# Kernel tuning notes

Measured on AMD Instinct MI355X. Metric: run time of the kernel, lower is better.

Reference implementation:

```python
import jax, jax.numpy as jnp
import numpy as np

D_MODEL = 1024
N_HEADS = 16
HEAD_DIM = D_MODEL // N_HEADS
THETA = 10000.0
NEG = -1e9


def apply_rope(x, positions, theta=THETA):
    # x: (B, H, S, d), positions: (B, 1, S)
    d = x.shape[-1]
    inv_freq = 1.0 / (theta ** (jnp.arange(0, d, 2, dtype=jnp.float32) / d))  # (d/2,)
    freqs = positions[..., None].astype(jnp.float32) * inv_freq  # (B, 1, S, d/2)
    cos, sin = jnp.cos(freqs), jnp.sin(freqs)
    xr = x.reshape(x.shape[:-1] + (d // 2, 2))
    xe, xo = xr[..., 0], xr[..., 1]
    rot = jnp.stack([xe * cos - xo * sin, xe * sin + xo * cos], axis=-1)
    return rot.reshape(x.shape)


def setup_inputs() -> dict:
    key = jax.random.key(0)
    ks = jax.random.split(key, 5)
    B, S = 2, 2048
    scale = 1.0 / np.sqrt(D_MODEL)
    return {
        "x": jax.random.normal(ks[0], (B, S, D_MODEL), dtype=jnp.float32),
        "wq": jax.random.normal(ks[1], (D_MODEL, D_MODEL), dtype=jnp.float32) * scale,
        "wk": jax.random.normal(ks[2], (D_MODEL, D_MODEL), dtype=jnp.float32) * scale,
        "wv": jax.random.normal(ks[3], (D_MODEL, D_MODEL), dtype=jnp.float32) * scale,
        "wo": jax.random.normal(ks[4], (D_MODEL, D_MODEL), dtype=jnp.float32) * scale,
        "token_positions": jnp.arange(S, dtype=jnp.int64),
    }


def reference(x, wq, wk, wv, wo, token_positions):
    B, S, D = x.shape
    H, d = N_HEADS, HEAD_DIM
    # QKV projections (module does x @ w.T)
    q = (x @ wq.T).reshape(B, S, H, d).transpose(0, 2, 1, 3)  # (B, H, S, d)
    k = (x @ wk.T).reshape(B, S, H, d).transpose(0, 2, 1, 3)
    v = (x @ wv.T).reshape(B, S, H, d).transpose(0, 2, 1, 3)
    pos = jnp.broadcast_to(token_positions[None, :], (B, S))[:, None, :]  # (B, 1, S)
    q = apply_rope(q, pos)
    k = apply_rope(k, pos)
    scores = jnp.einsum("bhqd,bhkd->bhqk", q, k) / jnp.sqrt(jnp.float32(d))
    causal = jnp.tril(jnp.ones((S, S), dtype=bool))
    scores = jnp.where(causal[None, None], scores, NEG)
    attn = jax.nn.softmax(scores, axis=-1)
    out = jnp.einsum("bhqk,bhkd->bhqd", attn, v)
    out = out.transpose(0, 2, 1, 3).reshape(B, S, D)
    return out @ wo.T
```

## Files before the change

### kernel.cpp

```cpp
#include <hip/hip_runtime.h>

typedef __bf16 bf16;
typedef __bf16 bf16x8 __attribute__((ext_vector_type(8)));
typedef __bf16 bf16x4 __attribute__((ext_vector_type(4)));
typedef float f32x4 __attribute__((ext_vector_type(4)));
typedef float f32x16 __attribute__((ext_vector_type(16)));
typedef float fx2 __attribute__((ext_vector_type(2)));

#define DEV static __device__ __forceinline__

constexpr int BB = 2, SS = 2048, DM = 1024, NH = 16, HD = 64;
constexpr int MTOT = BB * SS;
constexpr float LOG2E = 1.4426950408889634f;

constexpr size_t OFF_XB   = 0;
constexpr size_t OFF_WQKV = OFF_XB   + (size_t)MTOT * DM * 2;
constexpr size_t OFF_WO   = OFF_WQKV + (size_t)3 * DM * DM * 2;
constexpr size_t OFF_TAB  = OFF_WO   + (size_t)DM * DM * 2;
constexpr size_t OFF_Q    = OFF_TAB  + (size_t)SS * (HD/2) * 8;
constexpr size_t OFF_K    = OFF_Q    + (size_t)MTOT * DM * 2;
constexpr size_t OFF_VF   = OFF_K    + (size_t)MTOT * DM * 2;
constexpr size_t OFF_AO   = OFF_VF   + (size_t)MTOT * DM * 2;

typedef const __attribute__((address_space(1))) void gas_void;
typedef __attribute__((address_space(3))) void las_void;

DEV void gload16(const bf16* g, bf16* l) {
  __builtin_amdgcn_global_load_lds((gas_void*)g, (las_void*)l, 16, 0, 0);
}

DEV f32x4 mfma16(bf16x8 a, bf16x8 b, f32x4 c) {
  return __builtin_amdgcn_mfma_f32_16x16x32_bf16(a, b, c, 0, 0, 0);
}

DEV f32x16 mfma32(bf16x8 a, bf16x8 b, f32x16 c) {
  return __builtin_amdgcn_mfma_f32_32x32x16_bf16(a, b, c, 0, 0, 0);
}

DEV unsigned pack2(float a, float b) {
  union { bf16 h[2]; unsigned u; } cv;
  cv.h[0] = (bf16)a; cv.h[1] = (bf16)b;
  return cv.u;
}

__global__ void prep_kernel(const float* __restrict__ x, const float* __restrict__ wq,
    const float* __restrict__ wk, const float* __restrict__ wv, const float* __restrict__ wo,
    const int* __restrict__ pos, bf16* __restrict__ xb, bf16* __restrict__ wqkv,
    bf16* __restrict__ wob, fx2* __restrict__ tab) {
  const int NX4 = MTOT * DM / 4;
  const int NW4 = DM * DM / 4;
  const int TOTC = NX4 + 4 * NW4;
  const int NTAB = SS * (HD / 2);
  const int total = TOTC + NTAB;
  for (int i = blockIdx.x * blockDim.x + threadIdx.x; i < total; i += gridDim.x * blockDim.x) {
    if (i < TOTC) {
      const float* src; bf16* dst; int off;
      if (i < NX4) { src = x; dst = xb; off = i; }
      else {
        int i2 = i - NX4; int which = i2 >> 18; off = i2 & (NW4 - 1);
        src = which == 0 ? wq : which == 1 ? wk : which == 2 ? wv : wo;
        dst = which == 0 ? wqkv : which == 1 ? wqkv + DM * DM : which == 2 ? wqkv + 2 * DM * DM : wob;
      }
      float4 v = ((const float4*)src)[off];
      bf16x4 o4 = { (bf16)v.x, (bf16)v.y, (bf16)v.z, (bf16)v.w };
      ((bf16x4*)dst)[off] = o4;
    } else {
      int e = i - TOTC;
      int s = e >> 5, p = e & 31;
      float invf = __builtin_exp2f(-(float)p * (13.287712379549449f / 32.0f));
      float ang = (float)pos[s] * invf;
      fx2 cs; cs.x = cosf(ang); cs.y = sinf(ang);
      tab[e] = cs;
    }
  }
}

DEV void gemm_bt_128(const bf16* __restrict__ A, const bf16* __restrict__ Bw,
                     int rowA0, int rowB0, f32x4 (&acc)[4][4]) {
  __shared__ __align__(16) bf16 lA[128 * 32];
  __shared__ __align__(16) bf16 lB[128 * 32];
  const int t = threadIdx.x, w = t >> 6, lane = t & 63;
  const int wr = w >> 1, wc = w & 1, g = lane >> 4, c = lane & 15;
#pragma unroll
  for (int mi = 0; mi < 4; mi++)
#pragma unroll
    for (int ni = 0; ni < 4; ni++) acc[mi][ni] = (f32x4){0.f, 0.f, 0.f, 0.f};
  const bf16* ga = A + (size_t)(rowA0 + (t >> 2)) * DM + (t & 3) * 8;
  const bf16* gb = Bw + (size_t)(rowB0 + (t >> 2)) * DM + (t & 3) * 8;
  bf16* la = lA + w * 512;
  bf16* lb = lB + w * 512;
  const int arow = wr * 64 + c, brow = wc * 64 + c;
  for (int k0 = 0; k0 < DM; k0 += 32) {
    gload16(ga + k0,            la);
    gload16(ga + k0 + 64 * DM,  la + 2048);
    gload16(gb + k0,            lb);
    gload16(gb + k0 + 64 * DM,  lb + 2048);
    __syncthreads();
    bf16x8 af[4], bf_[4];
#pragma unroll
    for (int mi = 0; mi < 4; mi++) af[mi]  = *(const bf16x8*)(lA + (arow + mi * 16) * 32 + g * 8);
#pragma unroll
    for (int ni = 0; ni < 4; ni++) bf_[ni] = *(const bf16x8*)(lB + (brow + ni * 16) * 32 + g * 8);
#pragma unroll
    for (int mi = 0; mi < 4; mi++)
#pragma unroll
      for (int ni = 0; ni < 4; ni++)
        acc[mi][ni] = mfma16(af[mi], bf_[ni], acc[mi][ni]);
    __syncthreads();
  }
}

__global__ __launch_bounds__(256, 2) void qkv_kernel(const bf16* __restrict__ xb,
    const bf16* __restrict__ wqkv, const fx2* __restrict__ tab,
    bf16* __restrict__ Qb, bf16* __restrict__ Kb, bf16* __restrict__ VFb) {
  f32x4 acc[4][4];
  const int rowA0 = blockIdx.y * 128, rowB0 = blockIdx.x * 128;
  gemm_bt_128(xb, wqkv, rowA0, rowB0, acc);
  const int t = threadIdx.x, w = t >> 6, lane = t & 63;
  const int wr = w >> 1, wc = w & 1, g = lane >> 4, c = lane & 15;
  const int which = rowB0 >> 10;
#pragma unroll
  for (int mi = 0; mi < 4; mi++)
#pragma unroll
    for (int ni = 0; ni < 4; ni++) {
      const int ncol = rowB0 + wc * 64 + ni * 16 + c;
      const int nn = ncol & (DM - 1), h = nn >> 6, dd = nn & 63;
#pragma unroll
      for (int j = 0; j < 4; j++) {
        const int mrow = rowA0 + wr * 64 + mi * 16 + 4 * g + j;
        const int b = mrow >> 11, s = mrow & (SS - 1);
        float v = acc[mi][ni][j];
        if (which < 2) {
          float partner = __shfl_xor(v, 1);
          fx2 cs = tab[s * 32 + (dd >> 1)];
          v = v * cs.x + ((dd & 1) ? partner : -partner) * cs.y;
          bf16* dst = which == 0 ? Qb : Kb;
          dst[((size_t)((b * NH + h) * SS + s)) * HD + dd] = (bf16)v;
        } else {
          const int t2 = ((rowA0 & (SS - 1)) >> 6) + wr;
          const int e2 = (4 * g + j) & 7;
          const int lane2 = (dd & 31) + 32 * (g >> 1);
          VFb[(((((size_t)(b * NH + h) * 32 + t2) * 2 + (dd >> 5)) * 4 + mi) * 64 + lane2) * 8 + e2] = (bf16)v;
        }
      }
    }
}

__global__ __launch_bounds__(128, 2) void attn_kernel(const bf16* __restrict__ Q,
    const bf16* __restrict__ K, const bf16* __restrict__ VF, bf16* __restrict__ AO) {
  __shared__ __align__(16) unsigned char smem[32768];
  const int flat = blockIdx.x;
  const int flat2 = (flat & 7) * 128 + (flat >> 3);
  const int bh = flat2 >> 5;
  const int p = flat2 & 31;
  const int w = threadIdx.x >> 6;
  const int lane = threadIdx.x & 63;
  const int q31 = lane & 31, hi = lane >> 5;
  const bf16* Qp = Q + (size_t)bh * SS * HD;
  const bf16* Kp = K + (size_t)bh * SS * HD;
  const bf16* VFp = VF + (size_t)bh * SS * HD;
  const float SCL = 0.125f * LOG2E;
  const unsigned wbase = (unsigned)w * 16384;
  float* Om = (float*)(smem + 16384);
  float* Ml = (float*)(smem + 24576);
  float* Ll = (float*)(smem + 24576 + 128);

  const bf16* kSrcBase = Kp + (size_t)(lane >> 3) * HD + ((lane & 7) ^ (lane >> 3)) * 8;
  auto stageK = [&](int k0, unsigned koff) {
    const bf16* src = kSrcBase + (size_t)k0 * HD;
    bf16* dst = (bf16*)(smem + koff);
#pragma unroll
    for (int i = 0; i < 8; i++)
      gload16(src + i * 8 * HD, dst + i * 512);
  };

  auto run_chunk = [&](int qbase, int nt) {
    bf16x8 qb[4];
#pragma unroll
    for (int ds = 0; ds < 4; ds++) {
      bf16x8 xq = *(const bf16x8*)(Qp + (size_t)(qbase + q31) * HD + ds * 16 + hi * 8);
#pragma unroll
      for (int e = 0; e < 8; e++) xq[e] = (bf16)((float)xq[e] * SCL);
      qb[ds] = xq;
    }
    float m_r = -3.0e38f, lsum = 0.f;
    f32x16 o0, o1;
#pragma unroll
    for (int e = 0; e < 16; e++) { o0[e] = 0.f; o1[e] = 0.f; }

    unsigned cur = 0;
    if (w < nt) stageK(w * 64, wbase);
    for (int tv = w; tv < nt; tv += 2) {
      const int k0 = tv * 64;
      asm volatile("s_waitcnt vmcnt(0)" ::: "memory");
      __builtin_amdgcn_sched_barrier(0);
      f32x16 s0, s1;
#pragma unroll
      for (int e = 0; e < 16; e++) { s0[e] = 0.f; s1[e] = 0.f; }
      {
        const unsigned rowb0 = wbase + cur * 8192 + (unsigned)q31 * 128;
        const unsigned sw = (unsigned)(q31 & 7) << 4;
#pragma unroll
        for (int ds = 0; ds < 4; ds++) {
          const unsigned co = (((unsigned)(ds * 2 + hi)) << 4) ^ sw;
          bf16x8 kf0 = *(const bf16x8*)(smem + rowb0 + co);
          bf16x8 kf1 = *(const bf16x8*)(smem + rowb0 + 4096 + co);
          s0 = mfma32(kf0, qb[ds], s0);
          s1 = mfma32(kf1, qb[ds], s1);
        }
      }
      bf16x8 vf[2][4];
      {
        const bf16* vt = VFp + (size_t)(k0 >> 6) * 4096;
#pragma unroll
        for (int dt = 0; dt < 2; dt++)
#pragma unroll
          for (int ks = 0; ks < 4; ks++)
            vf[dt][ks] = *(const bf16x8*)(vt + (size_t)((dt * 4 + ks) * 64 + lane) * 8);
      }
      if (tv + 2 < nt) stageK((tv + 2) * 64, wbase + (cur ^ 1) * 8192);
      if (k0 + 63 > qbase) {
        const int qg = qbase + q31;
#pragma unroll
        for (int r = 0; r < 16; r++) {
          const int kg = k0 + (r & 3) + 8 * (r >> 2) + 4 * hi;
          if (kg > qg)      s0[r] = -1.0e30f;
          if (kg + 32 > qg) s1[r] = -1.0e30f;
        }
      }
      {
        float a[16];
#pragma unroll
        for (int r = 0; r < 16; r++) a[r] = fmaxf(s0[r], s1[r]);
#pragma unroll
        for (int d = 8; d > 0; d >>= 1)
#pragma unroll
          for (int r = 0; r < d; r++) a[r] = fmaxf(a[r], a[r + d]);
        const float pm = fmaxf(a[0], __shfl_xor(a[0], 32));
        if (__any(pm > m_r + 8.0f)) {
          const float mnew = fmaxf(m_r, pm);
          const float alpha = __builtin_exp2f(m_r - mnew);
          lsum *= alpha;
#pragma unroll
          for (int e = 0; e < 16; e++) { o0[e] *= alpha; o1[e] *= alpha; }
          m_r = mnew;
        }
        float b[16];
#pragma unroll
        for (int r = 0; r < 16; r++) {
          s0[r] = __builtin_exp2f(s0[r] - m_r);
          s1[r] = __builtin_exp2f(s1[r] - m_r);
          b[r] = s0[r] + s1[r];
        }
#pragma unroll
        for (int d = 8; d > 0; d >>= 1)
#pragma unroll
          for (int r = 0; r < d; r++) b[r] += b[r + d];
        lsum += b[0] + __shfl_xor(b[0], 32);
      }
      bf16x8 pf[4];
#pragma unroll
      for (int ks = 0; ks < 4; ks++) {
        const int rb = 8 * (ks & 1);
        float va0, va1, va2, va3, vb0, vb1, vb2, vb3;
        if (ks < 2) {
          va0 = s0[rb]; va1 = s0[rb + 1]; va2 = s0[rb + 2]; va3 = s0[rb + 3];
          vb0 = s0[rb + 4]; vb1 = s0[rb + 5]; vb2 = s0[rb + 6]; vb3 = s0[rb + 7];
        } else {
          va0 = s1[rb]; va1 = s1[rb + 1]; va2 = s1[rb + 2]; va3 = s1[rb + 3];
          vb0 = s1[rb + 4]; vb1 = s1[rb + 5]; vb2 = s1[rb + 6]; vb3 = s1[rb + 7];
        }
        const unsigned a01 = pack2(va0, va1), a23 = pack2(va2, va3);
        const unsigned b01 = pack2(vb0, vb1), b23 = pack2(vb2, vb3);
        const unsigned z1 = (unsigned)__shfl_xor((int)(hi ? a01 : b01), 32);
        const unsigned z2 = (unsigned)__shfl_xor((int)(hi ? a23 : b23), 32);
        union { unsigned u[4]; bf16x8 v; } cv;
        cv.u[0] = hi ? z1 : a01;
        cv.u[1] = hi ? z2 : a23;
        cv.u[2] = hi ? b01 : z1;
        cv.u[3] = hi ? b23 : z2;
        pf[ks] = cv.v;
      }
#pragma unroll
      for (int ks = 0; ks < 4; ks++) {
        o0 = mfma32(vf[0][ks], pf[ks], o0);
        o1 = mfma32(vf[1][ks], pf[ks], o1);
      }
      cur ^= 1;
    }
    __syncthreads();
    if (w) {
#pragma unroll
      for (int e = 0; e < 16; e++) {
        const int r = (e & 3) + 8 * (e >> 2) + 4 * hi;
        Om[r * 32 + q31] = o0[e];
        Om[(r + 32) * 32 + q31] = o1[e];
      }
      if (!hi) { Ml[q31] = m_r; Ll[q31] = lsum; }
    }
    __syncthreads();
    if (!w) {
      const float m1 = Ml[q31], l1 = Ll[q31];
      const float mm = fmaxf(m_r, m1);
      const float a0 = __builtin_exp2f(m_r - mm);
      const float a1 = __builtin_exp2f(m1 - mm);
      const float linv = 1.0f / (a0 * lsum + a1 * l1);
      const int b = bh >> 4, h = bh & 15;
      const size_t rowb = ((size_t)(b * SS + qbase + q31)) * DM + h * HD;
#pragma unroll
      for (int g2 = 0; g2 < 4; g2++) {
        bf16x4 w0v, w1v;
#pragma unroll
        for (int j = 0; j < 4; j++) {
          const int e = 4 * g2 + j;
          const int r = j + 8 * g2 + 4 * hi;
          w0v[j] = (bf16)((a0 * o0[e] + a1 * Om[r * 32 + q31]) * linv);
          w1v[j] = (bf16)((a0 * o1[e] + a1 * Om[(r + 32) * 32 + q31]) * linv);
        }
        *(bf16x4*)(AO + rowb +      8 * g2 + 4 * hi) = w0v;
        *(bf16x4*)(AO + rowb + 32 + 8 * g2 + 4 * hi) = w1v;
      }
    }
    __syncthreads();
  };

  run_chunk(p * 32, p / 2 + 1);
  const int ph = 63 - p;
  run_chunk(ph * 32, ph / 2 + 1);
}

__global__ __launch_bounds__(256, 2) void oproj_kernel(const bf16* __restrict__ AO,
    const bf16* __restrict__ wob, float* __restrict__ out) {
  f32x4 acc[4][4];
  const int rowA0 = blockIdx.y * 128, rowB0 = blockIdx.x * 128;
  gemm_bt_128(AO, wob, rowA0, rowB0, acc);
  const int t = threadIdx.x, w = t >> 6, lane = t & 63;
  const int wr = w >> 1, wc = w & 1, g = lane >> 4, c = lane & 15;
#pragma unroll
  for (int mi = 0; mi < 4; mi++)
#pragma unroll
    for (int ni = 0; ni < 4; ni++) {
      const int ncol = rowB0 + wc * 64 + ni * 16 + c;
#pragma unroll
      for (int j = 0; j < 4; j++) {
        const int mrow = rowA0 + wr * 64 + mi * 16 + 4 * g + j;
        out[(size_t)mrow * DM + ncol] = acc[mi][ni][j];
      }
    }
}

extern "C" void kernel_launch(void* const* d_in, const int* in_sizes, int n_in,
                              void* d_out, int out_size, void* d_ws, size_t ws_size,
                              hipStream_t stream) {
  const float* x  = (const float*)d_in[0];
  const float* wq = (const float*)d_in[1];
  const float* wk = (const float*)d_in[2];
  const float* wv = (const float*)d_in[3];
  const float* wo = (const float*)d_in[4];
  const int*   pos = (const int*)d_in[5];
  char* ws = (char*)d_ws;
  bf16* xb   = (bf16*)(ws + OFF_XB);
  bf16* wqkv = (bf16*)(ws + OFF_WQKV);
  bf16* wob  = (bf16*)(ws + OFF_WO);
  fx2*  tab  = (fx2*)(ws + OFF_TAB);
  bf16* Qb   = (bf16*)(ws + OFF_Q);
  bf16* Kb   = (bf16*)(ws + OFF_K);
  bf16* VFb  = (bf16*)(ws + OFF_VF);
  bf16* AOb  = (bf16*)(ws + OFF_AO);

  hipLaunchKernelGGL(prep_kernel, dim3(2048), dim3(256), 0, stream,
                     x, wq, wk, wv, wo, pos, xb, wqkv, wob, tab);
  hipLaunchKernelGGL(qkv_kernel, dim3(24, 32), dim3(256), 0, stream,
                     xb, wqkv, tab, Qb, Kb, VFb);
  hipLaunchKernelGGL(attn_kernel, dim3(1024), dim3(128), 0, stream,
                     Qb, Kb, VFb, AOb);
  hipLaunchKernelGGL(oproj_kernel, dim3(8, 32), dim3(256), 0, stream,
                     AOb, wob, (float*)d_out);
}
```

Measured before the change: 129.8 us.

## Store K in MFMA fragment layout and split attention keys across four waves

The QKV kernel now writes K in a pre-swizzled fragment layout, matching V, so the attention kernel loads K fragments straight from global memory into registers. This drops the LDS staging, double-buffering and vmcnt waits. The attention block grows from two to four waves, each taking every fourth key tile, and the final merge combines three partial softmax states through shared memory. The aim is more parallelism per query chunk and shorter per-wave loops, at the cost of exposed global-load latency without a software pipeline and a larger reduction step.

```diff
diff --git a/kernel.cpp b/kernel.cpp
--- a/kernel.cpp
+++ b/kernel.cpp
@@ -18,8 +18,8 @@
 constexpr size_t OFF_WO   = OFF_WQKV + (size_t)3 * DM * DM * 2;
 constexpr size_t OFF_TAB  = OFF_WO   + (size_t)DM * DM * 2;
 constexpr size_t OFF_Q    = OFF_TAB  + (size_t)SS * (HD/2) * 8;
-constexpr size_t OFF_K    = OFF_Q    + (size_t)MTOT * DM * 2;
-constexpr size_t OFF_VF   = OFF_K    + (size_t)MTOT * DM * 2;
+constexpr size_t OFF_KF   = OFF_Q    + (size_t)MTOT * DM * 2;
+constexpr size_t OFF_VF   = OFF_KF   + (size_t)MTOT * DM * 2;
 constexpr size_t OFF_AO   = OFF_VF   + (size_t)MTOT * DM * 2;
 
 typedef const __attribute__((address_space(1))) void gas_void;
@@ -112,7 +112,7 @@
 
 __global__ __launch_bounds__(256, 2) void qkv_kernel(const bf16* __restrict__ xb,
     const bf16* __restrict__ wqkv, const fx2* __restrict__ tab,
-    bf16* __restrict__ Qb, bf16* __restrict__ Kb, bf16* __restrict__ VFb) {
+    bf16* __restrict__ Qb, bf16* __restrict__ KFb, bf16* __restrict__ VFb) {
   f32x4 acc[4][4];
   const int rowA0 = blockIdx.y * 128, rowB0 = blockIdx.x * 128;
   gemm_bt_128(xb, wqkv, rowA0, rowB0, acc);
@@ -134,8 +134,14 @@
           float partner = __shfl_xor(v, 1);
           fx2 cs = tab[s * 32 + (dd >> 1)];
           v = v * cs.x + ((dd & 1) ? partner : -partner) * cs.y;
-          bf16* dst = which == 0 ? Qb : Kb;
-          dst[((size_t)((b * NH + h) * SS + s)) * HD + dd] = (bf16)v;
+          if (which == 0) {
+            Qb[((size_t)((b * NH + h) * SS + s)) * HD + dd] = (bf16)v;
+          } else {
+            const int kt = s >> 6, b32 = (s >> 5) & 1, l31 = s & 31;
+            const int ds2 = dd >> 4, hi2 = (dd >> 3) & 1, e2 = dd & 7;
+            const int lane2 = l31 + 32 * hi2;
+            KFb[((((size_t)(b * NH + h) * 32 + kt) * 8) + b32 * 4 + ds2) * 512 + lane2 * 8 + e2] = (bf16)v;
+          }
         } else {
           const int t2 = ((rowA0 & (SS - 1)) >> 6) + wr;
           const int e2 = (4 * g + j) & 7;
@@ -146,9 +152,11 @@
     }
 }
 
-__global__ __launch_bounds__(128, 2) void attn_kernel(const bf16* __restrict__ Q,
-    const bf16* __restrict__ K, const bf16* __restrict__ VF, bf16* __restrict__ AO) {
-  __shared__ __align__(16) unsigned char smem[32768];
+__global__ __launch_bounds__(256, 4) void attn_kernel(const bf16* __restrict__ Q,
+    const bf16* __restrict__ KF, const bf16* __restrict__ VF, bf16* __restrict__ AO) {
+  __shared__ float Om[3][2048];
+  __shared__ float Ml[3][32];
+  __shared__ float Ll[3][32];
   const int flat = blockIdx.x;
   const int flat2 = (flat & 7) * 128 + (flat >> 3);
   const int bh = flat2 >> 5;
@@ -157,22 +165,9 @@
   const int lane = threadIdx.x & 63;
   const int q31 = lane & 31, hi = lane >> 5;
   const bf16* Qp = Q + (size_t)bh * SS * HD;
-  const bf16* Kp = K + (size_t)bh * SS * HD;
+  const bf16* KFp = KF + (size_t)bh * SS * HD;
   const bf16* VFp = VF + (size_t)bh * SS * HD;
   const float SCL = 0.125f * LOG2E;
-  const unsigned wbase = (unsigned)w * 16384;
-  float* Om = (float*)(smem + 16384);
-  float* Ml = (float*)(smem + 24576);
-  float* Ll = (float*)(smem + 24576 + 128);
-
-  const bf16* kSrcBase = Kp + (size_t)(lane >> 3) * HD + ((lane & 7) ^ (lane >> 3)) * 8;
-  auto stageK = [&](int k0, unsigned koff) {
-    const bf16* src = kSrcBase + (size_t)k0 * HD;
-    bf16* dst = (bf16*)(smem + koff);
-#pragma unroll
-    for (int i = 0; i < 8; i++)
-      gload16(src + i * 8 * HD, dst + i * 512);
-  };
 
   auto run_chunk = [&](int qbase, int nt) {
     bf16x8 qb[4];
@@ -188,37 +183,30 @@
 #pragma unroll
     for (int e = 0; e < 16; e++) { o0[e] = 0.f; o1[e] = 0.f; }
 
-    unsigned cur = 0;
-    if (w < nt) stageK(w * 64, wbase);
-    for (int tv = w; tv < nt; tv += 2) {
+    for (int tv = w; tv < nt; tv += 4) {
       const int k0 = tv * 64;
-      asm volatile("s_waitcnt vmcnt(0)" ::: "memory");
-      __builtin_amdgcn_sched_barrier(0);
+      const bf16* kt = KFp + (size_t)tv * 4096;
+      const bf16* vt = VFp + (size_t)tv * 4096;
+      bf16x8 kf0[4], kf1[4];
+#pragma unroll
+      for (int ds = 0; ds < 4; ds++) {
+        kf0[ds] = *(const bf16x8*)(kt + (size_t)(ds * 64 + lane) * 8);
+        kf1[ds] = *(const bf16x8*)(kt + (size_t)((4 + ds) * 64 + lane) * 8);
+      }
+      bf16x8 vf[2][4];
+#pragma unroll
+      for (int dt = 0; dt < 2; dt++)
+#pragma unroll
+        for (int ks = 0; ks < 4; ks++)
+          vf[dt][ks] = *(const bf16x8*)(vt + (size_t)((dt * 4 + ks) * 64 + lane) * 8);
       f32x16 s0, s1;
 #pragma unroll
       for (int e = 0; e < 16; e++) { s0[e] = 0.f; s1[e] = 0.f; }
-      {
-        const unsigned rowb0 = wbase + cur * 8192 + (unsigned)q31 * 128;
-        const unsigned sw = (unsigned)(q31 & 7) << 4;
-#pragma unroll
-        for (int ds = 0; ds < 4; ds++) {
-          const unsigned co = (((unsigned)(ds * 2 + hi)) << 4) ^ sw;
-          bf16x8 kf0 = *(const bf16x8*)(smem + rowb0 + co);
-          bf16x8 kf1 = *(const bf16x8*)(smem + rowb0 + 4096 + co);
-          s0 = mfma32(kf0, qb[ds], s0);
-          s1 = mfma32(kf1, qb[ds], s1);
-        }
-      }
-      bf16x8 vf[2][4];
-      {
-        const bf16* vt = VFp + (size_t)(k0 >> 6) * 4096;
-#pragma unroll
-        for (int dt = 0; dt < 2; dt++)
-#pragma unroll
-          for (int ks = 0; ks < 4; ks++)
-            vf[dt][ks] = *(const bf16x8*)(vt + (size_t)((dt * 4 + ks) * 64 + lane) * 8);
-      }
-      if (tv + 2 < nt) stageK((tv + 2) * 64, wbase + (cur ^ 1) * 8192);
+#pragma unroll
+      for (int ds = 0; ds < 4; ds++) {
+        s0 = mfma32(kf0[ds], qb[ds], s0);
+        s1 = mfma32(kf1[ds], qb[ds], s1);
+      }
       if (k0 + 63 > qbase) {
         const int qg = qbase + q31;
 #pragma unroll
@@ -286,25 +274,32 @@
         o0 = mfma32(vf[0][ks], pf[ks], o0);
         o1 = mfma32(vf[1][ks], pf[ks], o1);
       }
-      cur ^= 1;
     }
     __syncthreads();
     if (w) {
 #pragma unroll
       for (int e = 0; e < 16; e++) {
         const int r = (e & 3) + 8 * (e >> 2) + 4 * hi;
-        Om[r * 32 + q31] = o0[e];
-        Om[(r + 32) * 32 + q31] = o1[e];
-      }
-      if (!hi) { Ml[q31] = m_r; Ll[q31] = lsum; }
+        Om[w - 1][r * 32 + q31] = o0[e];
+        Om[w - 1][(r + 32) * 32 + q31] = o1[e];
+      }
+      if (!hi) { Ml[w - 1][q31] = m_r; Ll[w - 1][q31] = lsum; }
     }
     __syncthreads();
     if (!w) {
-      const float m1 = Ml[q31], l1 = Ll[q31];
-      const float mm = fmaxf(m_r, m1);
-      const float a0 = __builtin_exp2f(m_r - mm);
-      const float a1 = __builtin_exp2f(m1 - mm);
-      const float linv = 1.0f / (a0 * lsum + a1 * l1);
+      float mi_[3];
+#pragma unroll
+      for (int i = 0; i < 3; i++) mi_[i] = Ml[i][q31];
+      float mm = fmaxf(fmaxf(m_r, mi_[0]), fmaxf(mi_[1], mi_[2]));
+      const float aS = __builtin_exp2f(m_r - mm);
+      float ai[3];
+      float L = aS * lsum;
+#pragma unroll
+      for (int i = 0; i < 3; i++) {
+        ai[i] = __builtin_exp2f(mi_[i] - mm);
+        L += ai[i] * Ll[i][q31];
+      }
+      const float linv = 1.0f / L;
       const int b = bh >> 4, h = bh & 15;
       const size_t rowb = ((size_t)(b * SS + qbase + q31)) * DM + h * HD;
 #pragma unroll
@@ -314,8 +309,15 @@
         for (int j = 0; j < 4; j++) {
           const int e = 4 * g2 + j;
           const int r = j + 8 * g2 + 4 * hi;
-          w0v[j] = (bf16)((a0 * o0[e] + a1 * Om[r * 32 + q31]) * linv);
-          w1v[j] = (bf16)((a0 * o1[e] + a1 * Om[(r + 32) * 32 + q31]) * linv);
+          float v0 = aS * o0[e];
+          float v1 = aS * o1[e];
+#pragma unroll
+          for (int i = 0; i < 3; i++) {
+            v0 += ai[i] * Om[i][r * 32 + q31];
+            v1 += ai[i] * Om[i][(r + 32) * 32 + q31];
+          }
+          w0v[j] = (bf16)(v0 * linv);
+          w1v[j] = (bf16)(v1 * linv);
         }
         *(bf16x4*)(AO + rowb +      8 * g2 + 4 * hi) = w0v;
         *(bf16x4*)(AO + rowb + 32 + 8 * g2 + 4 * hi) = w1v;
@@ -364,16 +366,16 @@
   bf16* wob  = (bf16*)(ws + OFF_WO);
   fx2*  tab  = (fx2*)(ws + OFF_TAB);
   bf16* Qb   = (bf16*)(ws + OFF_Q);
-  bf16* Kb   = (bf16*)(ws + OFF_K);
+  bf16* KFb  = (bf16*)(ws + OFF_KF);
   bf16* VFb  = (bf16*)(ws + OFF_VF);
   bf16* AOb  = (bf16*)(ws + OFF_AO);
 
   hipLaunchKernelGGL(prep_kernel, dim3(2048), dim3(256), 0, stream,
                      x, wq, wk, wv, wo, pos, xb, wqkv, wob, tab);
   hipLaunchKernelGGL(qkv_kernel, dim3(24, 32), dim3(256), 0, stream,
-                     xb, wqkv, tab, Qb, Kb, VFb);
-  hipLaunchKernelGGL(attn_kernel, dim3(1024), dim3(128), 0, stream,
-                     Qb, Kb, VFb, AOb);
+                     xb, wqkv, tab, Qb, KFb, VFb);
+  hipLaunchKernelGGL(attn_kernel, dim3(1024), dim3(256), 0, stream,
+                     Qb, KFb, VFb, AOb);
   hipLaunchKernelGGL(oproj_kernel, dim3(8, 32), dim3(256), 0, stream,
                      AOb, wob, (float*)d_out);
 }
```

After: 141.8 us. 1.09x slower.
